# Optimization experiments

Measured on AMD Instinct MI355X. Metric: run time of the kernel, lower is better.

## Reference

```python
import jax, jax.numpy as jnp
import numpy as np
from jax import lax

GAMMA = 0.99
CLIP_VALUE = 5.0
EPS = 1e-07

B, T = 1024, 8192


def setup_inputs() -> dict:
    key = jax.random.key(0)
    k1, k2, k3, k4 = jax.random.split(key, 4)
    return {
        "log_probs": jax.random.normal(k1, (B, T), dtype=jnp.float32),
        "logits": jax.random.normal(k2, (B, T, 1), dtype=jnp.float32),
        "weight": jax.random.uniform(k3, (B, T), dtype=jnp.float32),
        "baselines": jax.random.normal(k4, (B, T, 1), dtype=jnp.float32),
    }


def _discounted_reverse_cumsum(r2):
    # r2: [B, T]; c_t = r2_t + gamma * c_{t+1}  (reverse scan over time)
    def step(c, r):
        c = r + GAMMA * c
        return c, c

    _, cum = lax.scan(step, jnp.zeros(r2.shape[0], r2.dtype), r2.T, reverse=True)
    return cum.T  # [B, T]


def reference(log_probs, logits, weight, baselines):
    # rewards = log(sigmoid(logits) + EPS).squeeze(-1) * weight
    rewards = jnp.log(jax.nn.sigmoid(logits) + EPS)[..., 0] * weight
    # inner-loop term is k * weight[:, s] * rewards[:, s] -> weight applied again
    r2 = weight * rewards
    cumulative_rewards = _discounted_reverse_cumsum(r2)
    advantages = jnp.clip(weight * cumulative_rewards, -CLIP_VALUE, CLIP_VALUE)
    generator_objective = advantages * log_probs
    return (generator_objective, cumulative_rewards)
```

## Files before the change

### kernel.cpp

```cpp
#include <hip/hip_runtime.h>


#define T_LEN 8192
#define CHUNK 2048
#define NT 256
#define CSEG 8
#define GAMMA_F 0.99f
#define CLIP_F 5.0f
#define EPS_F 1e-7f

typedef float f32x4 __attribute__((ext_vector_type(4)));

constexpr double dgpow(int n) {
    double r = 1.0;
    for (int i = 0; i < n; ++i) r *= 0.99;
    return r;
}

__device__ __forceinline__ float r2f(float w, float x) {
    float s = 1.0f / (1.0f + __expf(-x));
    return w * w * __logf(s + EPS_F);
}

__global__ __launch_bounds__(NT)
void reinforce_kernel(const float* __restrict__ log_probs,
                      const float* __restrict__ logits,
                      const float* __restrict__ weight,
                      float* __restrict__ out,
                      long BT) {
    const int bid  = blockIdx.x;
    const int k    = bid & 7;
    const int j    = bid >> 3;
    const int chunk = j & 3;
    const int row   = (j >> 2) * 8 + k;

    const long rbase = (long)row * T_LEN;
    const long cbase = rbase + (long)chunk * CHUNK;
    const int tid  = threadIdx.x;
    const int lane = tid & 63;
    const int wave = tid >> 6;
    const int seg  = tid * CSEG;

    __shared__ float RED[4];
    __shared__ float WT[4];

    f32x4 hw, hx;
    if (chunk != 3) {
        const long hbase = cbase + CHUNK + (long)tid * 4;
        hw = *reinterpret_cast<const f32x4*>(weight + hbase);
        hx = *reinterpret_cast<const f32x4*>(logits + hbase);
    }
    const f32x4* w4  = reinterpret_cast<const f32x4*>(weight + cbase + seg);
    const f32x4* x4  = reinterpret_cast<const f32x4*>(logits + cbase + seg);
    const f32x4* lp4 = reinterpret_cast<const f32x4*>(log_probs + cbase + seg);
    f32x4 wq0 = w4[0], wq1 = w4[1];
    f32x4 xq0 = x4[0], xq1 = x4[1];
    f32x4 lq0 = lp4[0], lq1 = lp4[1];

    float r2[CSEG], wv[CSEG];
#pragma unroll
    for (int e = 0; e < 4; ++e) { wv[e] = wq0[e]; wv[4 + e] = wq1[e]; }
#pragma unroll
    for (int e = 0; e < 4; ++e) { r2[e] = r2f(wq0[e], xq0[e]); r2[4 + e] = r2f(wq1[e], xq1[e]); }

    float S = 0.0f;
#pragma unroll
    for (int jj = CSEG - 1; jj >= 0; --jj) S = r2[jj] + GAMMA_F * S;

    float X = S;
    {
        constexpr float G8   = (float)dgpow(8);
        constexpr float G16  = (float)dgpow(16);
        constexpr float G32  = (float)dgpow(32);
        constexpr float G64  = (float)dgpow(64);
        constexpr float G128 = (float)dgpow(128);
        constexpr float G256 = (float)dgpow(256);
        float t;
        t = __shfl_down(X, 1, 64);  if (lane + 1  < 64) X += G8   * t;
        t = __shfl_down(X, 2, 64);  if (lane + 2  < 64) X += G16  * t;
        t = __shfl_down(X, 4, 64);  if (lane + 4  < 64) X += G32  * t;
        t = __shfl_down(X, 8, 64);  if (lane + 8  < 64) X += G64  * t;
        t = __shfl_down(X, 16, 64); if (lane + 16 < 64) X += G128 * t;
        t = __shfl_down(X, 32, 64); if (lane + 32 < 64) X += G256 * t;
    }
    float Ex = __shfl_down(X, 1, 64);
    if (lane == 63) Ex = 0.0f;

    if (chunk != 3) {
        float h0 = r2f(hw[0], hx[0]), h1 = r2f(hw[1], hx[1]);
        float h2 = r2f(hw[2], hx[2]), h3 = r2f(hw[3], hx[3]);
        float hS = h0 + GAMMA_F * (h1 + GAMMA_F * (h2 + GAMMA_F * h3));
        const float L2G4 = 4.0f * -0.014499569695f;
        float part = exp2f((float)tid * L2G4) * hS;
#pragma unroll
        for (int off = 1; off < 64; off <<= 1)
            part += __shfl_xor(part, off, 64);
        if (lane == 0) RED[wave] = part;
    }
    if (lane == 0) WT[wave] = X;

    __syncthreads();

    float c_in = (chunk != 3) ? (RED[0] + RED[1] + RED[2] + RED[3]) : 0.0f;

    constexpr float G512  = (float)dgpow(512);
    constexpr float G1024 = (float)dgpow(1024);
    constexpr float G1536 = (float)dgpow(1536);
    float WC;
    if (wave == 3)      WC = c_in;
    else if (wave == 2) WC = WT[3] + G512 * c_in;
    else if (wave == 1) WC = WT[2] + G512 * WT[3] + G1024 * c_in;
    else                WC = WT[1] + G512 * WT[2] + G1024 * WT[3] + G1536 * c_in;

    const float L2G8 = 8.0f * -0.014499569695f;
    float K = Ex + exp2f((float)(63 - lane) * L2G8) * WC;

    f32x4* go4 = reinterpret_cast<f32x4*>(out + cbase + seg);
    f32x4* c4  = reinterpret_cast<f32x4*>(out + BT + cbase + seg);
    float lps[CSEG];
#pragma unroll
    for (int e = 0; e < 4; ++e) { lps[e] = lq0[e]; lps[4 + e] = lq1[e]; }

    float c = K;
#pragma unroll
    for (int q = CSEG / 4 - 1; q >= 0; --q) {
        f32x4 cq, gq;
#pragma unroll
        for (int e = 3; e >= 0; --e) {
            c = r2[4 * q + e] + GAMMA_F * c;
            cq[e] = c;
            float adv = fminf(fmaxf(wv[4 * q + e] * c, -CLIP_F), CLIP_F);
            gq[e] = adv * lps[4 * q + e];
        }
        c4[q]  = cq;
        go4[q] = gq;
    }
}

extern "C" void kernel_launch(void* const* d_in, const int* in_sizes, int n_in,
                              void* d_out, int out_size, void* d_ws, size_t ws_size,
                              hipStream_t stream) {
    const float* log_probs = (const float*)d_in[0];
    const float* logits    = (const float*)d_in[1];
    const float* weight    = (const float*)d_in[2];
    long BT = (long)in_sizes[0];
    int B = (int)(BT / T_LEN);
    int nblocks = B * (T_LEN / CHUNK);
    reinforce_kernel<<<nblocks, NT, 0, stream>>>(log_probs, logits, weight, (float*)d_out, BT);
}
```

Baseline: 31.58 us.

## Make each wave scan an independent 1024-element segment with its own halo

Each wave now owns a 1024-element segment of a row, with 16 elements per thread, and estimates its carry-in from its own 1024-element look-ahead halo. This removes the block-wide __syncthreads and the shared-memory combination of wave totals that the old 2048-element chunk design needed. Each block covers half a row, so the grid is half as large. The cost is more redundant halo reads of weight and logits (one halo per 1024 elements instead of per 2048) and more registers per thread.

```diff
diff --git a/kernel.cpp b/kernel.cpp
--- a/kernel.cpp
+++ b/kernel.cpp
@@ -2,12 +2,11 @@
 
 
 #define T_LEN 8192
-#define CHUNK 2048
 #define NT 256
-#define CSEG 8
 #define GAMMA_F 0.99f
 #define CLIP_F 5.0f
 #define EPS_F 1e-7f
+#define L2G 0.0144995696951151f
 
 typedef float f32x4 __attribute__((ext_vector_type(4)));
 
@@ -31,109 +30,100 @@
     const int bid  = blockIdx.x;
     const int k    = bid & 7;
     const int j    = bid >> 3;
-    const int chunk = j & 3;
-    const int row   = (j >> 2) * 8 + k;
+    const int half = j & 1;
+    const int row  = (j >> 1) * 8 + k;
+
+    const int wave = threadIdx.x >> 6;
+    const int lane = threadIdx.x & 63;
+    const int gc   = half * 4 + wave;
 
     const long rbase = (long)row * T_LEN;
-    const long cbase = rbase + (long)chunk * CHUNK;
-    const int tid  = threadIdx.x;
-    const int lane = tid & 63;
-    const int wave = tid >> 6;
-    const int seg  = tid * CSEG;
+    const long lbase = rbase + (long)gc * 1024 + lane * 16;
 
-    __shared__ float RED[4];
-    __shared__ float WT[4];
+    const f32x4* w4 = reinterpret_cast<const f32x4*>(weight + lbase);
+    const f32x4* x4 = reinterpret_cast<const f32x4*>(logits + lbase);
+    const f32x4* l4 = reinterpret_cast<const f32x4*>(log_probs + lbase);
 
-    f32x4 hw, hx;
-    if (chunk != 3) {
-        const long hbase = cbase + CHUNK + (long)tid * 4;
-        hw = *reinterpret_cast<const f32x4*>(weight + hbase);
-        hx = *reinterpret_cast<const f32x4*>(logits + hbase);
+    const bool has_halo = (gc != 7);
+
+    f32x4 wq[4], xq[4], lq[4], hw[4], hx[4];
+#pragma unroll
+    for (int q = 0; q < 4; ++q) { wq[q] = w4[q]; xq[q] = x4[q]; }
+    if (has_halo) {
+        const f32x4* hw4 = reinterpret_cast<const f32x4*>(weight + lbase + 1024);
+        const f32x4* hx4 = reinterpret_cast<const f32x4*>(logits + lbase + 1024);
+#pragma unroll
+        for (int q = 0; q < 4; ++q) { hw[q] = hw4[q]; hx[q] = hx4[q]; }
     }
-    const f32x4* w4  = reinterpret_cast<const f32x4*>(weight + cbase + seg);
-    const f32x4* x4  = reinterpret_cast<const f32x4*>(logits + cbase + seg);
-    const f32x4* lp4 = reinterpret_cast<const f32x4*>(log_probs + cbase + seg);
-    f32x4 wq0 = w4[0], wq1 = w4[1];
-    f32x4 xq0 = x4[0], xq1 = x4[1];
-    f32x4 lq0 = lp4[0], lq1 = lp4[1];
+#pragma unroll
+    for (int q = 0; q < 4; ++q) lq[q] = l4[q];
 
-    float r2[CSEG], wv[CSEG];
+    float r2[16];
 #pragma unroll
-    for (int e = 0; e < 4; ++e) { wv[e] = wq0[e]; wv[4 + e] = wq1[e]; }
+    for (int q = 0; q < 4; ++q)
 #pragma unroll
-    for (int e = 0; e < 4; ++e) { r2[e] = r2f(wq0[e], xq0[e]); r2[4 + e] = r2f(wq1[e], xq1[e]); }
+        for (int e = 0; e < 4; ++e)
+            r2[4 * q + e] = r2f(wq[q][e], xq[q][e]);
 
     float S = 0.0f;
 #pragma unroll
-    for (int jj = CSEG - 1; jj >= 0; --jj) S = r2[jj] + GAMMA_F * S;
+    for (int jj = 15; jj >= 0; --jj) S = r2[jj] + GAMMA_F * S;
 
     float X = S;
     {
-        constexpr float G8   = (float)dgpow(8);
         constexpr float G16  = (float)dgpow(16);
         constexpr float G32  = (float)dgpow(32);
         constexpr float G64  = (float)dgpow(64);
         constexpr float G128 = (float)dgpow(128);
         constexpr float G256 = (float)dgpow(256);
+        constexpr float G512 = (float)dgpow(512);
         float t;
-        t = __shfl_down(X, 1, 64);  if (lane + 1  < 64) X += G8   * t;
-        t = __shfl_down(X, 2, 64);  if (lane + 2  < 64) X += G16  * t;
-        t = __shfl_down(X, 4, 64);  if (lane + 4  < 64) X += G32  * t;
-        t = __shfl_down(X, 8, 64);  if (lane + 8  < 64) X += G64  * t;
-        t = __shfl_down(X, 16, 64); if (lane + 16 < 64) X += G128 * t;
-        t = __shfl_down(X, 32, 64); if (lane + 32 < 64) X += G256 * t;
+        t = __shfl_down(X, 1, 64);  if (lane + 1  < 64) X += G16  * t;
+        t = __shfl_down(X, 2, 64);  if (lane + 2  < 64) X += G32  * t;
+        t = __shfl_down(X, 4, 64);  if (lane + 4  < 64) X += G64  * t;
+        t = __shfl_down(X, 8, 64);  if (lane + 8  < 64) X += G128 * t;
+        t = __shfl_down(X, 16, 64); if (lane + 16 < 64) X += G256 * t;
+        t = __shfl_down(X, 32, 64); if (lane + 32 < 64) X += G512 * t;
     }
     float Ex = __shfl_down(X, 1, 64);
     if (lane == 63) Ex = 0.0f;
 
-    if (chunk != 3) {
-        float h0 = r2f(hw[0], hx[0]), h1 = r2f(hw[1], hx[1]);
-        float h2 = r2f(hw[2], hx[2]), h3 = r2f(hw[3], hx[3]);
-        float hS = h0 + GAMMA_F * (h1 + GAMMA_F * (h2 + GAMMA_F * h3));
-        const float L2G4 = 4.0f * -0.014499569695f;
-        float part = exp2f((float)tid * L2G4) * hS;
+    float c_in = 0.0f;
+    if (has_halo) {
+        float h2[16];
+#pragma unroll
+        for (int q = 0; q < 4; ++q)
+#pragma unroll
+            for (int e = 0; e < 4; ++e)
+                h2[4 * q + e] = r2f(hw[q][e], hx[q][e]);
+        float hS = 0.0f;
+#pragma unroll
+        for (int jj = 15; jj >= 0; --jj) hS = h2[jj] + GAMMA_F * hS;
+        float part = exp2f((float)(lane << 4) * -L2G) * hS;
 #pragma unroll
         for (int off = 1; off < 64; off <<= 1)
             part += __shfl_xor(part, off, 64);
-        if (lane == 0) RED[wave] = part;
+        c_in = part;
     }
-    if (lane == 0) WT[wave] = X;
 
-    __syncthreads();
+    float K = Ex + exp2f((float)((63 - lane) << 4) * -L2G) * c_in;
 
-    float c_in = (chunk != 3) ? (RED[0] + RED[1] + RED[2] + RED[3]) : 0.0f;
-
-    constexpr float G512  = (float)dgpow(512);
-    constexpr float G1024 = (float)dgpow(1024);
-    constexpr float G1536 = (float)dgpow(1536);
-    float WC;
-    if (wave == 3)      WC = c_in;
-    else if (wave == 2) WC = WT[3] + G512 * c_in;
-    else if (wave == 1) WC = WT[2] + G512 * WT[3] + G1024 * c_in;
-    else                WC = WT[1] + G512 * WT[2] + G1024 * WT[3] + G1536 * c_in;
-
-    const float L2G8 = 8.0f * -0.014499569695f;
-    float K = Ex + exp2f((float)(63 - lane) * L2G8) * WC;
-
-    f32x4* go4 = reinterpret_cast<f32x4*>(out + cbase + seg);
-    f32x4* c4  = reinterpret_cast<f32x4*>(out + BT + cbase + seg);
-    float lps[CSEG];
-#pragma unroll
-    for (int e = 0; e < 4; ++e) { lps[e] = lq0[e]; lps[4 + e] = lq1[e]; }
+    f32x4* go = reinterpret_cast<f32x4*>(out + lbase);
+    f32x4* co = reinterpret_cast<f32x4*>(out + BT + lbase);
 
     float c = K;
 #pragma unroll
-    for (int q = CSEG / 4 - 1; q >= 0; --q) {
+    for (int q = 3; q >= 0; --q) {
         f32x4 cq, gq;
 #pragma unroll
         for (int e = 3; e >= 0; --e) {
             c = r2[4 * q + e] + GAMMA_F * c;
             cq[e] = c;
-            float adv = fminf(fmaxf(wv[4 * q + e] * c, -CLIP_F), CLIP_F);
-            gq[e] = adv * lps[4 * q + e];
+            float adv = fminf(fmaxf(wq[q][e] * c, -CLIP_F), CLIP_F);
+            gq[e] = adv * lq[q][e];
         }
-        c4[q]  = cq;
-        go4[q] = gq;
+        co[q] = cq;
+        go[q] = gq;
     }
 }
 
@@ -144,7 +134,6 @@
     const float* logits    = (const float*)d_in[1];
     const float* weight    = (const float*)d_in[2];
     long BT = (long)in_sizes[0];
-    int B = (int)(BT / T_LEN);
-    int nblocks = B * (T_LEN / CHUNK);
+    int nblocks = (int)(BT / 4096);
     reinforce_kernel<<<nblocks, NT, 0, stream>>>(log_probs, logits, weight, (float*)d_out, BT);
 }
```

Measured after the change: 37.30 us. 18.1% more time.
